# Kernel tuning notes

Hardware: AMD Instinct MI355X
Metric: run time of the kernel (lower is better)

The kernel has to match this reference:

```python
import jax, jax.numpy as jnp
import numpy as np

Z_DIM = 2  # state dimension is hard-coded (fc1: Linear(2, H), fc3: Linear(H, 2))


def _mlp(z, W1, b1, W2, b2, W3, b3):
    # torch.nn.Linear: y = x @ W.T + b
    h = jax.nn.elu(z @ W1.T + b1)
    h = jax.nn.elu(h @ W2.T + b2)
    return h @ W3.T + b3


def setup_inputs() -> dict:
    key = jax.random.key(0)
    ks = jax.random.split(key, 8)
    B, H = 1_000_000, 64
    s_in = 1.0 / np.sqrt(Z_DIM)
    s_h = 1.0 / np.sqrt(H)
    u = lambda k, shp, s: jax.random.uniform(k, shp, jnp.float32, -s, s)
    return {
        "t": jax.random.normal(ks[0], (1,), jnp.float32),
        "z_and_logp": jax.random.normal(ks[1], (B, Z_DIM + 1), jnp.float32),
        "W1": u(ks[2], (H, Z_DIM), s_in),
        "b1": u(ks[3], (H,), s_in),
        "W2": u(ks[4], (H, H), s_h),
        "b2": u(ks[5], (H,), s_h),
        "W3": u(ks[6], (Z_DIM, H), s_h),
        "b3": u(ks[7], (Z_DIM,), s_h),
    }


def reference(t, z_and_logp, W1, b1, W2, b2, W3, b3):
    # t is an unused time argument (ODE solver interface).
    z = z_and_logp[:, :Z_DIM]  # [B, 2]; logp column is not used in forward
    f = lambda x: _mlp(x, W1, b1, W2, b2, W3, b3)

    # Exact Jacobian trace via forward-mode JVPs with unit tangents (Z_DIM=2,
    # so this small fixed loop mirrors the per-dim autograd loop in torch).
    dz_dt = None
    trace = jnp.zeros(z.shape[0], dtype=z.dtype)
    for i in range(Z_DIM):
        e = jnp.zeros_like(z).at[:, i].set(1.0)
        out, jz = jax.jvp(f, (z,), (e,))
        if dz_dt is None:
            dz_dt = out
        trace = trace + jz[:, i]

    dlogp_dt = -trace[:, None]  # [B, 1]
    return jnp.concatenate([dz_dt, dlogp_dt], axis=1)  # [B, 3]
```

## Files before the change

kernel.cpp:

```cpp
#include <hip/hip_runtime.h>
#include <hip/hip_fp16.h>


typedef _Float16 f16x8 __attribute__((ext_vector_type(8)));
typedef _Float16 f16x2 __attribute__((ext_vector_type(2)));
typedef float    f32x4 __attribute__((ext_vector_type(4)));

static __device__ __forceinline__ f16x8 exp2_h8(f16x8 t) {
    f16x8 e;
#pragma unroll
    for (int p = 0; p < 4; ++p) {
        f16x2 t2 = {t[2*p], t[2*p+1]};
        __half2 r = h2exp2(__builtin_bit_cast(__half2, t2));
        f16x2 e2 = __builtin_bit_cast(f16x2, r);
        e[2*p] = e2[0]; e[2*p+1] = e2[1];
    }
    return e;
}

static __device__ __forceinline__ f16x2 exp2_h2(f16x2 t) {
    __half2 r = h2exp2(__builtin_bit_cast(__half2, t));
    return __builtin_bit_cast(f16x2, r);
}

static __device__ __forceinline__ f16x2 cvtpk(float a, float b) {
    return __builtin_bit_cast(f16x2, __builtin_amdgcn_cvt_pkrtz(a, b));
}

static __device__ __forceinline__ f16x8 bcast8(float z) {
    _Float16 h = (_Float16)z;
    f16x8 v = {h, h, h, h, h, h, h, h};
    return v;
}

__global__ __launch_bounds__(256) __attribute__((amdgpu_waves_per_eu(2, 2)))
void odefunc_mfma(const float* __restrict__ zin,
                  const float* __restrict__ W1, const float* __restrict__ b1,
                  const float* __restrict__ W2, const float* __restrict__ b2,
                  const float* __restrict__ W3, const float* __restrict__ b3,
                  float* __restrict__ out, int B, int ntiles)
{
    const float L2E  = 1.442695040888963f;
    const float RL2E = 0.6931471805599453f;

    __shared__ _Float16 sH[192];
    __shared__ f32x4    sC[48];

    const int lane = threadIdx.x & 63;
    const int quad = lane >> 4;
    const int col  = lane & 15;

    if (threadIdx.x < 64) {
        int i = threadIdx.x;
        sH[i]       = (_Float16)(W1[2*i]     * L2E);
        sH[64 + i]  = (_Float16)(W1[2*i + 1] * L2E);
        sH[128 + i] = (_Float16)(b1[i]       * L2E);
        float* s = (float*)sC;
        s[i]       = b2[i] * L2E;
        s[64 + i]  = W3[i]      * RL2E;
        s[128 + i] = W3[64 + i] * RL2E;
    }

    const int wid    = blockIdx.x * (blockDim.x >> 6) + (threadIdx.x >> 6);
    const int nwaves = gridDim.x * (blockDim.x >> 6);

    f16x8 aW2[4][2], aG[4][2];
#pragma unroll
    for (int mt = 0; mt < 4; ++mt) {
        const int k = mt * 16 + col;
        const float ck = W3[k], dk = W3[64 + k];
#pragma unroll
        for (int jt = 0; jt < 2; ++jt) {
            const float* p = W2 + k * 64 + jt * 32 + quad * 8;
#pragma unroll
            for (int jj = 0; jj < 8; ++jj) {
                int j = jt * 32 + quad * 8 + jj;
                float w2 = p[jj];
                aW2[mt][jt][jj] = (_Float16)w2;
                aG[mt][jt][jj]  = (_Float16)(w2 * fmaf(ck, W1[2*j], dk * W1[2*j+1]));
            }
        }
    }

    const float b30 = b3[0], b31 = b3[1];
    const f32x4 zero4 = {0.f, 0.f, 0.f, 0.f};
    const _Float16 hl2e = (_Float16)L2E;
    const _Float16 h0   = (_Float16)0.0f;
    const f16x8 zero8 = {h0,h0,h0,h0,h0,h0,h0,h0};
    const f16x8 l2e8  = {hl2e,hl2e,hl2e,hl2e,hl2e,hl2e,hl2e,hl2e};
    const f16x8 ml2e8 = {-hl2e,-hl2e,-hl2e,-hl2e,-hl2e,-hl2e,-hl2e,-hl2e};
    const f16x2 zero2 = {h0, h0};
    const f16x2 l2e2  = {hl2e, hl2e};
    const f16x2 ml2e2 = {-hl2e, -hl2e};

    __syncthreads();

    f16x8 cw0[2], cw1[2], cbb[2];
#pragma unroll
    for (int jt = 0; jt < 2; ++jt) {
        int j0 = jt * 32 + quad * 8;
        cw0[jt] = *(const f16x8*)(sH + j0);
        cw1[jt] = *(const f16x8*)(sH + j0 + 64);
        cbb[jt] = *(const f16x8*)(sH + j0 + 128);
    }
    f32x4 cb2[4];
    f16x2 cw30h[4][2], cw31h[4][2];
#pragma unroll
    for (int mt = 0; mt < 4; ++mt) {
        int k4 = mt * 4 + quad;
        cb2[mt] = sC[k4];
        f32x4 w30 = sC[k4 + 16];
        f32x4 w31 = sC[k4 + 32];
        cw30h[mt][0] = cvtpk(w30[0], w30[1]);
        cw30h[mt][1] = cvtpk(w30[2], w30[3]);
        cw31h[mt][0] = cvtpk(w31[0], w31[1]);
        cw31h[mt][1] = cvtpk(w31[2], w31[3]);
    }

    const int lload = lane < 48 ? lane : 47;
    int tp = wid;
    float zv[3] = {0.f, 0.f, 0.f};
#pragma unroll
    for (int t = 0; t < 3; ++t) {
        int tt = 3 * tp + t;
        if (tt < ntiles) zv[t] = zin[tt * 48 + lload];
    }

    for (; 3 * tp < ntiles; tp += nwaves) {
        float zvn[3];
#pragma unroll
        for (int t = 0; t < 3; ++t) {
            int tt = 3 * (tp + nwaves) + t;
            zvn[t] = zin[(tt < ntiles ? tt : 0) * 48 + lload];
        }

        f16x8 z08[3], z18[3];
#pragma unroll
        for (int t = 0; t < 3; ++t) {
            z08[t] = bcast8(__shfl(zv[t], 3 * col));
            z18[t] = bcast8(__shfl(zv[t], 3 * col + 1));
        }

        f16x8 Bh[3][2], Be[3][2];
#pragma unroll
        for (int jt = 0; jt < 2; ++jt) {
#pragma unroll
            for (int t = 0; t < 3; ++t) {
                f16x8 a = __builtin_elementwise_fma(cw0[jt], z08[t],
                          __builtin_elementwise_fma(cw1[jt], z18[t], cbb[jt]));
                f16x8 e = exp2_h8(__builtin_elementwise_min(a, zero8));
                Bh[t][jt] = __builtin_elementwise_max(a,
                            __builtin_elementwise_fma(l2e8, e, ml2e8));
                Be[t][jt] = e;
            }
        }

        f32x4 aH[3][4], aT[3][4];
#pragma unroll
        for (int mt = 0; mt < 4; ++mt) {
#pragma unroll
            for (int t = 0; t < 3; ++t) {
                aH[t][mt] = __builtin_amdgcn_mfma_f32_16x16x32_f16(aW2[mt][0], Bh[t][0], cb2[mt], 0, 0, 0);
                aH[t][mt] = __builtin_amdgcn_mfma_f32_16x16x32_f16(aW2[mt][1], Bh[t][1], aH[t][mt], 0, 0, 0);
                aT[t][mt] = __builtin_amdgcn_mfma_f32_16x16x32_f16(aG[mt][0], Be[t][0], zero4, 0, 0, 0);
                aT[t][mt] = __builtin_amdgcn_mfma_f32_16x16x32_f16(aG[mt][1], Be[t][1], aT[t][mt], 0, 0, 0);
            }
        }

        f16x2 o0[3] = {zero2, zero2, zero2};
        f16x2 o1[3] = {zero2, zero2, zero2};
        f16x2 tr[3] = {zero2, zero2, zero2};
#pragma unroll
        for (int mt = 0; mt < 4; ++mt) {
#pragma unroll
            for (int p = 0; p < 2; ++p) {
                f16x2 w30p = cw30h[mt][p], w31p = cw31h[mt][p];
#pragma unroll
                for (int t = 0; t < 3; ++t) {
                    f16x2 ah = cvtpk(aH[t][mt][2*p], aH[t][mt][2*p+1]);
                    f16x2 at = cvtpk(aT[t][mt][2*p], aT[t][mt][2*p+1]);
                    f16x2 e  = exp2_h2(__builtin_elementwise_min(ah, zero2));
                    f16x2 hh = __builtin_elementwise_max(ah,
                               __builtin_elementwise_fma(l2e2, e, ml2e2));
                    o0[t] = __builtin_elementwise_fma(w30p, hh, o0[t]);
                    o1[t] = __builtin_elementwise_fma(w31p, hh, o1[t]);
                    tr[t] = __builtin_elementwise_fma(e, at, tr[t]);
                }
            }
        }

#pragma unroll
        for (int t = 0; t < 3; ++t) {
            float o0f = (float)o0[t][0] + (float)o0[t][1];
            float o1f = (float)o1[t][0] + (float)o1[t][1];
            float trf = (float)tr[t][0] + (float)tr[t][1];
            o0f += __shfl_xor(o0f, 16); o0f += __shfl_xor(o0f, 32);
            o1f += __shfl_xor(o1f, 16); o1f += __shfl_xor(o1f, 32);
            trf += __shfl_xor(trf, 16); trf += __shfl_xor(trf, 32);
            int tt = 3 * tp + t;
            int row = tt * 16 + col;
            if (lane < 16 && tt < ntiles && row < B) {
                out[3 * row + 0] = o0f + b30;
                out[3 * row + 1] = o1f + b31;
                out[3 * row + 2] = -trf;
            }
        }

#pragma unroll
        for (int t = 0; t < 3; ++t) zv[t] = zvn[t];
    }
}

extern "C" void kernel_launch(void* const* d_in, const int* in_sizes, int n_in,
                              void* d_out, int out_size, void* d_ws, size_t ws_size,
                              hipStream_t stream) {
    const float* zin = (const float*)d_in[1];
    const float* W1  = (const float*)d_in[2];
    const float* b1  = (const float*)d_in[3];
    const float* W2  = (const float*)d_in[4];
    const float* b2  = (const float*)d_in[5];
    const float* W3  = (const float*)d_in[6];
    const float* b3  = (const float*)d_in[7];
    float* out = (float*)d_out;

    int B = in_sizes[1] / 3;
    int ntiles = (B + 15) / 16;
    int grid = 1024;
    odefunc_mfma<<<grid, 256, 0, stream>>>(zin, W1, b1, W2, b2, W3, b3,
                                           out, B, ntiles);
}
```

Baseline: 116.3 us.

## Software-pipeline tiles so MFMA of next tile overlaps ELU epilogue of current

Replaces the three-tiles-per-iteration batch with a two-stage software pipeline. Each wave computes layer-1 and the MFMAs for tile n+1 while it finishes the layer-2 ELU, output dot products and trace for tile n, and it prefetches z two tiles ahead. The final cross-lane reductions now shuffle packed fp16 pairs, so fewer shuffles are needed, at some cost in precision. The grid is halved to 512 blocks, which gives each wave more tiles to amortise pipeline startup. The first unguarded load assumes wid < ntiles, and fp16 reductions may lose accuracy.

```diff
diff --git a/kernel.cpp b/kernel.cpp
--- a/kernel.cpp
+++ b/kernel.cpp
@@ -27,10 +27,9 @@
     return __builtin_bit_cast(f16x2, __builtin_amdgcn_cvt_pkrtz(a, b));
 }
 
-static __device__ __forceinline__ f16x8 bcast8(float z) {
-    _Float16 h = (_Float16)z;
-    f16x8 v = {h, h, h, h, h, h, h, h};
-    return v;
+static __device__ __forceinline__ f16x2 shfl_xor_h2(f16x2 v, int m) {
+    int u = __shfl_xor(__builtin_bit_cast(int, v), m);
+    return __builtin_bit_cast(f16x2, u);
 }
 
 __global__ __launch_bounds__(256) __attribute__((amdgpu_waves_per_eu(2, 2)))
@@ -62,7 +61,7 @@
     }
 
     const int wid    = blockIdx.x * (blockDim.x >> 6) + (threadIdx.x >> 6);
-    const int nwaves = gridDim.x * (blockDim.x >> 6);
+    const int nw     = gridDim.x * (blockDim.x >> 6);
 
     f16x8 aW2[4][2], aG[4][2];
 #pragma unroll
@@ -118,96 +117,80 @@
     }
 
     const int lload = lane < 48 ? lane : 47;
-    int tp = wid;
-    float zv[3] = {0.f, 0.f, 0.f};
-#pragma unroll
-    for (int t = 0; t < 3; ++t) {
-        int tt = 3 * tp + t;
-        if (tt < ntiles) zv[t] = zin[tt * 48 + lload];
-    }
-
-    for (; 3 * tp < ntiles; tp += nwaves) {
-        float zvn[3];
-#pragma unroll
-        for (int t = 0; t < 3; ++t) {
-            int tt = 3 * (tp + nwaves) + t;
-            zvn[t] = zin[(tt < ntiles ? tt : 0) * 48 + lload];
-        }
-
-        f16x8 z08[3], z18[3];
-#pragma unroll
-        for (int t = 0; t < 3; ++t) {
-            z08[t] = bcast8(__shfl(zv[t], 3 * col));
-            z18[t] = bcast8(__shfl(zv[t], 3 * col + 1));
-        }
-
-        f16x8 Bh[3][2], Be[3][2];
+
+    struct Acc { f32x4 H[4]; f32x4 T[4]; };
+    Acc acc0, acc1;
+
+    auto tile_compute = [&](float zvt, Acc& ac) {
+        float z0 = __shfl(zvt, 3 * col), z1 = __shfl(zvt, 3 * col + 1);
+        const _Float16 z0h = (_Float16)z0, z1h = (_Float16)z1;
+        const f16x8 z08 = {z0h,z0h,z0h,z0h,z0h,z0h,z0h,z0h};
+        const f16x8 z18 = {z1h,z1h,z1h,z1h,z1h,z1h,z1h,z1h};
+        f16x8 Bh[2], Be[2];
 #pragma unroll
         for (int jt = 0; jt < 2; ++jt) {
-#pragma unroll
-            for (int t = 0; t < 3; ++t) {
-                f16x8 a = __builtin_elementwise_fma(cw0[jt], z08[t],
-                          __builtin_elementwise_fma(cw1[jt], z18[t], cbb[jt]));
-                f16x8 e = exp2_h8(__builtin_elementwise_min(a, zero8));
-                Bh[t][jt] = __builtin_elementwise_max(a,
-                            __builtin_elementwise_fma(l2e8, e, ml2e8));
-                Be[t][jt] = e;
+            f16x8 a = __builtin_elementwise_fma(cw0[jt], z08,
+                      __builtin_elementwise_fma(cw1[jt], z18, cbb[jt]));
+            f16x8 e = exp2_h8(__builtin_elementwise_min(a, zero8));
+            Bh[jt] = __builtin_elementwise_max(a,
+                     __builtin_elementwise_fma(l2e8, e, ml2e8));
+            Be[jt] = e;
+        }
+#pragma unroll
+        for (int mt = 0; mt < 4; ++mt) {
+            ac.H[mt] = __builtin_amdgcn_mfma_f32_16x16x32_f16(aW2[mt][0], Bh[0], cb2[mt], 0, 0, 0);
+            ac.H[mt] = __builtin_amdgcn_mfma_f32_16x16x32_f16(aW2[mt][1], Bh[1], ac.H[mt], 0, 0, 0);
+            ac.T[mt] = __builtin_amdgcn_mfma_f32_16x16x32_f16(aG[mt][0], Be[0], zero4, 0, 0, 0);
+            ac.T[mt] = __builtin_amdgcn_mfma_f32_16x16x32_f16(aG[mt][1], Be[1], ac.T[mt], 0, 0, 0);
+        }
+    };
+
+    auto tile_finish = [&](Acc& ac, int tt) {
+        f16x2 o02 = zero2, o12 = zero2, tr2 = zero2;
+#pragma unroll
+        for (int mt = 0; mt < 4; ++mt) {
+#pragma unroll
+            for (int p = 0; p < 2; ++p) {
+                f16x2 ah = cvtpk(ac.H[mt][2*p], ac.H[mt][2*p+1]);
+                f16x2 at = cvtpk(ac.T[mt][2*p], ac.T[mt][2*p+1]);
+                f16x2 e  = exp2_h2(__builtin_elementwise_min(ah, zero2));
+                f16x2 hh = __builtin_elementwise_max(ah,
+                           __builtin_elementwise_fma(l2e2, e, ml2e2));
+                o02 = __builtin_elementwise_fma(cw30h[mt][p], hh, o02);
+                o12 = __builtin_elementwise_fma(cw31h[mt][p], hh, o12);
+                tr2 = __builtin_elementwise_fma(e, at, tr2);
             }
         }
-
-        f32x4 aH[3][4], aT[3][4];
-#pragma unroll
-        for (int mt = 0; mt < 4; ++mt) {
-#pragma unroll
-            for (int t = 0; t < 3; ++t) {
-                aH[t][mt] = __builtin_amdgcn_mfma_f32_16x16x32_f16(aW2[mt][0], Bh[t][0], cb2[mt], 0, 0, 0);
-                aH[t][mt] = __builtin_amdgcn_mfma_f32_16x16x32_f16(aW2[mt][1], Bh[t][1], aH[t][mt], 0, 0, 0);
-                aT[t][mt] = __builtin_amdgcn_mfma_f32_16x16x32_f16(aG[mt][0], Be[t][0], zero4, 0, 0, 0);
-                aT[t][mt] = __builtin_amdgcn_mfma_f32_16x16x32_f16(aG[mt][1], Be[t][1], aT[t][mt], 0, 0, 0);
-            }
-        }
-
-        f16x2 o0[3] = {zero2, zero2, zero2};
-        f16x2 o1[3] = {zero2, zero2, zero2};
-        f16x2 tr[3] = {zero2, zero2, zero2};
-#pragma unroll
-        for (int mt = 0; mt < 4; ++mt) {
-#pragma unroll
-            for (int p = 0; p < 2; ++p) {
-                f16x2 w30p = cw30h[mt][p], w31p = cw31h[mt][p];
-#pragma unroll
-                for (int t = 0; t < 3; ++t) {
-                    f16x2 ah = cvtpk(aH[t][mt][2*p], aH[t][mt][2*p+1]);
-                    f16x2 at = cvtpk(aT[t][mt][2*p], aT[t][mt][2*p+1]);
-                    f16x2 e  = exp2_h2(__builtin_elementwise_min(ah, zero2));
-                    f16x2 hh = __builtin_elementwise_max(ah,
-                               __builtin_elementwise_fma(l2e2, e, ml2e2));
-                    o0[t] = __builtin_elementwise_fma(w30p, hh, o0[t]);
-                    o1[t] = __builtin_elementwise_fma(w31p, hh, o1[t]);
-                    tr[t] = __builtin_elementwise_fma(e, at, tr[t]);
-                }
-            }
-        }
-
-#pragma unroll
-        for (int t = 0; t < 3; ++t) {
-            float o0f = (float)o0[t][0] + (float)o0[t][1];
-            float o1f = (float)o1[t][0] + (float)o1[t][1];
-            float trf = (float)tr[t][0] + (float)tr[t][1];
-            o0f += __shfl_xor(o0f, 16); o0f += __shfl_xor(o0f, 32);
-            o1f += __shfl_xor(o1f, 16); o1f += __shfl_xor(o1f, 32);
-            trf += __shfl_xor(trf, 16); trf += __shfl_xor(trf, 32);
-            int tt = 3 * tp + t;
-            int row = tt * 16 + col;
-            if (lane < 16 && tt < ntiles && row < B) {
-                out[3 * row + 0] = o0f + b30;
-                out[3 * row + 1] = o1f + b31;
-                out[3 * row + 2] = -trf;
-            }
-        }
-
-#pragma unroll
-        for (int t = 0; t < 3; ++t) zv[t] = zvn[t];
+        f16x2 po = { (_Float16)(o02[0] + o02[1]), (_Float16)(o12[0] + o12[1]) };
+        f16x2 pt = { (_Float16)(tr2[0] + tr2[1]), h0 };
+        po += shfl_xor_h2(po, 16);  po += shfl_xor_h2(po, 32);
+        pt += shfl_xor_h2(pt, 16);  pt += shfl_xor_h2(pt, 32);
+        int row = tt * 16 + col;
+        if (lane < 16 && row < B) {
+            out[3 * row + 0] = (float)po[0] + b30;
+            out[3 * row + 1] = (float)po[1] + b31;
+            out[3 * row + 2] = -(float)pt[0];
+        }
+    };
+
+    int t = wid;
+    float zcur = zin[t * 48 + lload];
+    int tn0 = t + nw;
+    float znext = zin[(tn0 < ntiles ? tn0 : 0) * 48 + lload];
+    tile_compute(zcur, acc0);
+
+    while (true) {
+        int t2 = t + 2 * nw;
+        zcur = zin[(t2 < ntiles ? t2 : 0) * 48 + lload];
+        tile_compute(znext, acc1);
+        tile_finish(acc0, t);
+        if (t + nw >= ntiles) break;
+        int t3 = t + 3 * nw;
+        znext = zin[(t3 < ntiles ? t3 : 0) * 48 + lload];
+        tile_compute(zcur, acc0);
+        tile_finish(acc1, t + nw);
+        if (t2 >= ntiles) break;
+        t = t2;
     }
 }
 
@@ -225,7 +208,7 @@
 
     int B = in_sizes[1] / 3;
     int ntiles = (B + 15) / 16;
-    int grid = 1024;
+    int grid = 512;
     odefunc_mfma<<<grid, 256, 0, stream>>>(zin, W1, b1, W2, b2, W3, b3,
                                            out, B, ntiles);
 }
```

Result: no change. 115.3 us (-0.9%).
